# Optimization experiments

Hardware: AMD Instinct MI355X
Metric: run time of the kernel (lower is better)

Reference implementation:

```python
import jax, jax.numpy as jnp
import numpy as np

B, N, K = 2, 1280, 48
C_NODE, C_EDGE, C_OUT = 384, 128, 128
C_BIAS = C_NODE // 2          # 192 (node_dilation=2)
HID = 2 * C_BIAS + C_EDGE     # 512
LN_EPS = 1e-5


def setup_inputs() -> dict:
    key = jax.random.key(0)
    ks = jax.random.split(key, 13)
    w = lambda k, shape: (jax.random.normal(k, shape, jnp.float32) * 0.02)
    return {
        "node_emb": jax.random.normal(ks[0], (B, N, C_NODE), jnp.float32),
        "edge_emb": jax.random.normal(ks[1], (B, N, K, C_EDGE), jnp.float32),
        "E_idx": jax.random.randint(ks[2], (B, N, K), 0, N),
        "Wi": w(ks[3], (C_NODE, C_BIAS)), "bi": jnp.zeros((C_BIAS,), jnp.float32),
        "W1": w(ks[4], (HID, HID)), "b1": jnp.zeros((HID,), jnp.float32),
        "W2": w(ks[5], (HID, HID)), "b2": jnp.zeros((HID,), jnp.float32),
        "Wf": w(ks[6], (HID, C_OUT)), "bf": jnp.zeros((C_OUT,), jnp.float32),
        "gamma": jnp.ones((C_OUT,), jnp.float32),
        "beta": jnp.zeros((C_OUT,), jnp.float32),
    }


def reference(node_emb, edge_emb, E_idx, Wi, bi, W1, b1, W2, b2, Wf, bf, gamma, beta):
    # initial_embed: [B, N, C_NODE] -> [B, N, C_BIAS]
    n = node_emb @ Wi + bi
    # edge_bias[b,i,k] = concat(n[b,i], n[b, E_idx[b,i,k]])  (tile + gather_edges fused)
    nbr = jax.vmap(lambda v, e: v[e])(n, E_idx)                     # [B, N, K, C_BIAS]
    slf = jnp.broadcast_to(n[:, :, None, :], nbr.shape)             # [B, N, K, C_BIAS]
    x = jnp.concatenate([edge_emb, slf, nbr], axis=-1)              # [B, N, K, HID]
    h = jax.nn.relu(x @ W1 + b1)
    h = jax.nn.relu(h @ W2 + b2)
    # final_layer on residual sum, then LayerNorm
    y = (h + x) @ Wf + bf                                           # [B, N, K, C_OUT]
    mu = jnp.mean(y, axis=-1, keepdims=True)
    var = jnp.mean((y - mu) ** 2, axis=-1, keepdims=True)
    return (y - mu) * jax.lax.rsqrt(var + LN_EPS) * gamma + beta
```

## Files before the change

### kernel.cpp

```cpp
#include <hip/hip_runtime.h>
#include <stdint.h>

#define BB    2
#define NN    1280
#define KK    48
#define CN    384
#define CE    128
#define CB    192
#define HID   512
#define CO    128
#define MM    (BB*NN*KK)
#define CH    (MM/2)

typedef __bf16 bf16x8 __attribute__((ext_vector_type(8)));
typedef float  f32x4  __attribute__((ext_vector_type(4)));
typedef unsigned short u16x8 __attribute__((ext_vector_type(8)));

__device__ __forceinline__ unsigned short f2bf(float f) {
  unsigned int i = __builtin_bit_cast(unsigned int, f);
  unsigned int r = (i + 0x7fffu + ((i >> 16) & 1u)) >> 16;
  return (unsigned short)r;
}
__device__ __forceinline__ float bf2f(unsigned short u) {
  unsigned int v = ((unsigned int)u) << 16;
  return __builtin_bit_cast(float, v);
}

__device__ __forceinline__ void gload_lds16(const void* g, void* l) {
  __builtin_amdgcn_global_load_lds(
      (const __attribute__((address_space(1))) void*)g,
      (__attribute__((address_space(3))) void*)l, 16, 0, 0);
}

__device__ __forceinline__ void mfma_tiles(const char* ldsA, const char* ldsB,
                                           int l, int wm, int wn,
                                           f32x4 (&acc)[4][4]) {
#pragma unroll
  for (int kk = 0; kk < 2; ++kk) {
    bf16x8 av[4], bv[4];
#pragma unroll
    for (int t = 0; t < 4; ++t) {
      const int ra = wm * 64 + t * 16 + (l & 15);
      const int ca = (kk * 4 + (l >> 4)) ^ (ra & 7);
      av[t] = *(const bf16x8*)(ldsA + ra * 128 + ca * 16);
      const int rb = wn * 64 + t * 16 + (l & 15);
      const int cb = (kk * 4 + (l >> 4)) ^ (rb & 7);
      bv[t] = *(const bf16x8*)(ldsB + rb * 128 + cb * 16);
    }
#pragma unroll
    for (int mt = 0; mt < 4; ++mt)
#pragma unroll
      for (int nt = 0; nt < 4; ++nt)
        acc[mt][nt] = __builtin_amdgcn_mfma_f32_16x16x32_bf16(av[mt], bv[nt], acc[mt][nt], 0, 0, 0);
  }
}

__global__ void k_transpose_cast(const float* __restrict__ in,
                                 unsigned short* __restrict__ out,
                                 int R, int C) {
  __shared__ float tile[32][33];
  const int c0 = blockIdx.x * 32, r0 = blockIdx.y * 32;
  const int tx = threadIdx.x, ty = threadIdx.y;
#pragma unroll
  for (int dy = 0; dy < 32; dy += 8)
    tile[ty + dy][tx] = in[(size_t)(r0 + ty + dy) * C + c0 + tx];
  __syncthreads();
#pragma unroll
  for (int dy = 0; dy < 32; dy += 8)
    out[(size_t)(c0 + ty + dy) * R + r0 + tx] = f2bf(tile[tx][ty + dy]);
}

__global__ void k_node(const float* __restrict__ node,
                       const float* __restrict__ Wi,
                       const float* __restrict__ bi,
                       unsigned short* __restrict__ nbuf) {
  __shared__ float row[CN];
  const int blk = blockIdx.x;
  const float* src = node + (size_t)blk * CN;
  for (int c = threadIdx.x; c < CN; c += CB) row[c] = src[c];
  __syncthreads();
  const int t = threadIdx.x;
  float acc = bi[t];
#pragma unroll 8
  for (int c = 0; c < CN; ++c) acc += row[c] * Wi[(size_t)c * CB + t];
  nbuf[(size_t)blk * CB + t] = f2bf(acc);
}

__global__ __launch_bounds__(256, 2)
void k_gemm1(const float* __restrict__ edge,
             const unsigned short* __restrict__ nbuf,
             const int* __restrict__ eidx,
             const unsigned short* __restrict__ Wt,
             const float* __restrict__ bias,
             unsigned short* __restrict__ out,
             int mbase, int b) {
  __shared__ char lds[32768];
  char* ldsA = lds;
  char* ldsB = lds + 16384;
  const int flat = blockIdx.x;
  const int xcd = flat & 7;
  const int p = flat >> 3;
  const int m0 = (xcd * 60 + (p >> 2)) * 128;
  const int n0 = (p & 3) * 128;
  const int tid = threadIdx.x;
  const int l = tid & 63;
  const int w = tid >> 6;
  const int wm = w >> 1, wn = w & 1;
  const int sr = l >> 3, pc = l & 7;
  const int lc = pc ^ sr;

  int rr[4], big[4], nbrg[4];
  size_t mg[4];
#pragma unroll
  for (int ii = 0; ii < 4; ++ii) {
    const int r = (w * 4 + ii) * 8 + sr;
    rr[ii] = r;
    const int m = mbase + m0 + r;
    mg[ii] = (size_t)m;
    big[ii] = m / KK;
    nbrg[ii] = b * NN + eidx[m];
  }

  f32x4 acc[4][4];
#pragma unroll
  for (int i = 0; i < 4; ++i)
#pragma unroll
    for (int j = 0; j < 4; ++j) acc[i][j] = (f32x4){0.f, 0.f, 0.f, 0.f};

#pragma unroll
  for (int k0 = 0; k0 < HID; k0 += 64) {
    uint4 rga[4];
    if (k0 < 128) {
#pragma unroll
      for (int ii = 0; ii < 4; ++ii) {
        const float4* ep = (const float4*)(edge + mg[ii] * CE + k0 + lc * 8);
        float4 x0 = ep[0], x1 = ep[1];
        u16x8 pk;
        pk[0] = f2bf(x0.x); pk[1] = f2bf(x0.y); pk[2] = f2bf(x0.z); pk[3] = f2bf(x0.w);
        pk[4] = f2bf(x1.x); pk[5] = f2bf(x1.y); pk[6] = f2bf(x1.z); pk[7] = f2bf(x1.w);
        rga[ii] = __builtin_bit_cast(uint4, pk);
      }
    }
    __syncthreads();
#pragma unroll
    for (int ii = 0; ii < 4; ++ii) {
      const int i = w * 4 + ii;
      gload_lds16(Wt + (size_t)(n0 + rr[ii]) * HID + k0 + lc * 8, ldsB + i * 1024);
      if (k0 < 128) {
        *(uint4*)(ldsA + i * 1024 + l * 16) = rga[ii];
      } else if (k0 < 320) {
        gload_lds16(nbuf + (size_t)big[ii] * CB + (k0 - 128) + lc * 8, ldsA + i * 1024);
      } else {
        gload_lds16(nbuf + (size_t)nbrg[ii] * CB + (k0 - 320) + lc * 8, ldsA + i * 1024);
      }
    }
    __syncthreads();
    mfma_tiles(ldsA, ldsB, l, wm, wn, acc);
  }

  __syncthreads();
  unsigned short* tile = (unsigned short*)lds;
  const int q = l >> 4, cc = l & 15;
#pragma unroll
  for (int nt = 0; nt < 4; ++nt) {
    const int col = wn * 64 + nt * 16 + cc;
    const float bvv = bias[n0 + col];
    const int cn = col >> 3, cb = col & 7;
#pragma unroll
    for (int mt = 0; mt < 4; ++mt) {
      const int r0_ = wm * 64 + mt * 16 + q * 4;
#pragma unroll
      for (int r = 0; r < 4; ++r) {
        float v = acc[mt][nt][r] + bvv;
        v = v > 0.f ? v : 0.f;
        const int row = r0_ + r;
        tile[row * 128 + ((cn ^ (row & 7)) << 3) + cb] = f2bf(v);
      }
    }
  }
  __syncthreads();
#pragma unroll
  for (int i = 0; i < 8; ++i) {
    const int c = i * 256 + tid;
    const int row = c >> 4, cn = c & 15;
    u16x8 vv = *(const u16x8*)(tile + row * 128 + ((cn ^ (row & 7)) << 3));
    *(u16x8*)(out + (size_t)(m0 + row) * HID + n0 + cn * 8) = vv;
  }
}

__global__ __launch_bounds__(256, 2)
void k_gemm2(const unsigned short* __restrict__ A,
             const unsigned short* __restrict__ Wt,
             const float* __restrict__ bias,
             const float* __restrict__ edge,
             const unsigned short* __restrict__ nbuf,
             const int* __restrict__ eidx,
             unsigned short* __restrict__ out,
             int mbase, int b) {
  __shared__ char lds[32768];
  char* ldsA = lds;
  char* ldsB = lds + 16384;
  const int flat = blockIdx.x;
  const int xcd = flat & 7;
  const int p = flat >> 3;
  const int m0 = (xcd * 60 + (p >> 2)) * 128;
  const int n0 = (p & 3) * 128;
  const int tid = threadIdx.x;
  const int l = tid & 63;
  const int w = tid >> 6;
  const int wm = w >> 1, wn = w & 1;
  const int sr = l >> 3, pc = l & 7;
  const int lc = pc ^ sr;

  f32x4 acc[4][4];
#pragma unroll
  for (int i = 0; i < 4; ++i)
#pragma unroll
    for (int j = 0; j < 4; ++j) acc[i][j] = (f32x4){0.f, 0.f, 0.f, 0.f};

#pragma unroll
  for (int k0 = 0; k0 < HID; k0 += 64) {
    __syncthreads();
#pragma unroll
    for (int ii = 0; ii < 4; ++ii) {
      const int i = w * 4 + ii;
      const int r = i * 8 + sr;
      gload_lds16(A  + (size_t)(m0 + r) * HID + k0 + lc * 8, ldsA + i * 1024);
      gload_lds16(Wt + (size_t)(n0 + r) * HID + k0 + lc * 8, ldsB + i * 1024);
    }
    __syncthreads();
    mfma_tiles(ldsA, ldsB, l, wm, wn, acc);
  }

  __syncthreads();
  unsigned short* tile = (unsigned short*)lds;
  const int q = l >> 4, cc = l & 15;
#pragma unroll
  for (int nt = 0; nt < 4; ++nt) {
    const int col = wn * 64 + nt * 16 + cc;
    const float bvv = bias[n0 + col];
    const int cn = col >> 3, cb = col & 7;
#pragma unroll
    for (int mt = 0; mt < 4; ++mt) {
      const int r0_ = wm * 64 + mt * 16 + q * 4;
#pragma unroll
      for (int r = 0; r < 4; ++r) {
        float v = acc[mt][nt][r] + bvv;
        v = v > 0.f ? v : 0.f;
        const int row = r0_ + r;
        tile[row * 128 + ((cn ^ (row & 7)) << 3) + cb] = f2bf(v);
      }
    }
  }
  __syncthreads();
#pragma unroll
  for (int i = 0; i < 8; ++i) {
    const int c = i * 256 + tid;
    const int row = c >> 4, cn = c & 15;
    u16x8 vv = *(const u16x8*)(tile + row * 128 + ((cn ^ (row & 7)) << 3));
    const int m = mbase + m0 + row;
    float rv[8];
    if (n0 == 0) {
      const float4* ep = (const float4*)(edge + (size_t)m * CE + cn * 8);
      float4 x0 = ep[0], x1 = ep[1];
      rv[0] = x0.x; rv[1] = x0.y; rv[2] = x0.z; rv[3] = x0.w;
      rv[4] = x1.x; rv[5] = x1.y; rv[6] = x1.z; rv[7] = x1.w;
    } else if (n0 == 128) {
      u16x8 xv = *(const u16x8*)(nbuf + (size_t)(m / KK) * CB + cn * 8);
#pragma unroll
      for (int j = 0; j < 8; ++j) rv[j] = bf2f(xv[j]);
    } else if (n0 == 256) {
      u16x8 xv;
      if (cn < 8) {
        xv = *(const u16x8*)(nbuf + (size_t)(m / KK) * CB + 128 + cn * 8);
      } else {
        const int e = eidx[m];
        xv = *(const u16x8*)(nbuf + (size_t)(b * NN + e) * CB + cn * 8 - 64);
      }
#pragma unroll
      for (int j = 0; j < 8; ++j) rv[j] = bf2f(xv[j]);
    } else {
      const int e = eidx[m];
      u16x8 xv = *(const u16x8*)(nbuf + (size_t)(b * NN + e) * CB + 64 + cn * 8);
#pragma unroll
      for (int j = 0; j < 8; ++j) rv[j] = bf2f(xv[j]);
    }
#pragma unroll
    for (int j = 0; j < 8; ++j) vv[j] = f2bf(bf2f(vv[j]) + rv[j]);
    *(u16x8*)(out + (size_t)(m0 + row) * HID + n0 + cn * 8) = vv;
  }
}

__global__ __launch_bounds__(256, 2)
void k_final(const unsigned short* __restrict__ A,
             const unsigned short* __restrict__ Wft,
             const float* __restrict__ bias,
             const float* __restrict__ gamma,
             const float* __restrict__ beta,
             float* __restrict__ out) {
  __shared__ char lds[32768];
  char* ldsA = lds;
  char* ldsB = lds + 16384;
  const int m0 = blockIdx.x * 128;
  const int tid = threadIdx.x;
  const int l = tid & 63;
  const int w = tid >> 6;
  const int sr = l >> 3, pc = l & 7;
  const int lc = pc ^ sr;

  f32x4 acc[2][8];
#pragma unroll
  for (int i = 0; i < 2; ++i)
#pragma unroll
    for (int j = 0; j < 8; ++j) acc[i][j] = (f32x4){0.f, 0.f, 0.f, 0.f};

#pragma unroll
  for (int k0 = 0; k0 < HID; k0 += 64) {
    __syncthreads();
#pragma unroll
    for (int ii = 0; ii < 4; ++ii) {
      const int i = w * 4 + ii;
      const int r = i * 8 + sr;
      gload_lds16(A   + (size_t)(m0 + r) * HID + k0 + lc * 8, ldsA + i * 1024);
      gload_lds16(Wft + (size_t)r * HID + k0 + lc * 8,        ldsB + i * 1024);
    }
    __syncthreads();
#pragma unroll
    for (int kk = 0; kk < 2; ++kk) {
      bf16x8 av[2], bv[8];
#pragma unroll
      for (int t = 0; t < 2; ++t) {
        const int ra = w * 32 + t * 16 + (l & 15);
        const int ca = (kk * 4 + (l >> 4)) ^ (ra & 7);
        av[t] = *(const bf16x8*)(ldsA + ra * 128 + ca * 16);
      }
#pragma unroll
      for (int t = 0; t < 8; ++t) {
        const int rb = t * 16 + (l & 15);
        const int cb = (kk * 4 + (l >> 4)) ^ (rb & 7);
        bv[t] = *(const bf16x8*)(ldsB + rb * 128 + cb * 16);
      }
#pragma unroll
      for (int mt = 0; mt < 2; ++mt)
#pragma unroll
        for (int nt = 0; nt < 8; ++nt)
          acc[mt][nt] = __builtin_amdgcn_mfma_f32_16x16x32_bf16(av[mt], bv[nt], acc[mt][nt], 0, 0, 0);
    }
  }

  const int q = l >> 4, cc = l & 15;
  float gg[8], bb[8], bs[8];
#pragma unroll
  for (int j = 0; j < 8; ++j) {
    const int col = j * 16 + cc;
    gg[j] = gamma[col];
    bb[j] = beta[col];
    bs[j] = bias[col];
  }
#pragma unroll
  for (int mt = 0; mt < 2; ++mt) {
#pragma unroll
    for (int r = 0; r < 4; ++r) {
      float s = 0.f, ss = 0.f;
#pragma unroll
      for (int j = 0; j < 8; ++j) {
        const float v = acc[mt][j][r] + bs[j];
        acc[mt][j][r] = v;
        s += v;
        ss += v * v;
      }
#pragma unroll
      for (int mk = 1; mk < 16; mk <<= 1) {
        s  += __shfl_xor(s, mk, 64);
        ss += __shfl_xor(ss, mk, 64);
      }
      const float mu = s * (1.f / 128.f);
      const float var = ss * (1.f / 128.f) - mu * mu;
      const float rstd = rsqrtf(var + 1e-5f);
      const int row = m0 + w * 32 + mt * 16 + q * 4 + r;
#pragma unroll
      for (int j = 0; j < 8; ++j) {
        const float v = (acc[mt][j][r] - mu) * rstd * gg[j] + bb[j];
        out[(size_t)row * CO + j * 16 + cc] = v;
      }
    }
  }
}

#define O_N    ((size_t)0)
#define O_WT1  ((size_t)0x100000)
#define O_WT2  (O_WT1 + (size_t)0x80000)
#define O_WFT  (O_WT2 + (size_t)0x80000)
#define O_H1   ((size_t)0x300000)
#define O_A    (O_H1 + (size_t)CH * HID * 2)

extern "C" void kernel_launch(void* const* d_in, const int* in_sizes, int n_in,
                              void* d_out, int out_size, void* d_ws, size_t ws_size,
                              hipStream_t stream) {
  const float* node  = (const float*)d_in[0];
  const float* edge  = (const float*)d_in[1];
  const int*   eidx  = (const int*)d_in[2];
  const float* Wi    = (const float*)d_in[3];
  const float* bi    = (const float*)d_in[4];
  const float* W1    = (const float*)d_in[5];
  const float* b1    = (const float*)d_in[6];
  const float* W2    = (const float*)d_in[7];
  const float* b2    = (const float*)d_in[8];
  const float* Wf    = (const float*)d_in[9];
  const float* bfv   = (const float*)d_in[10];
  const float* gamma = (const float*)d_in[11];
  const float* beta  = (const float*)d_in[12];
  float* out = (float*)d_out;

  char* ws = (char*)d_ws;
  unsigned short* nbuf = (unsigned short*)(ws + O_N);
  unsigned short* Wt1  = (unsigned short*)(ws + O_WT1);
  unsigned short* Wt2  = (unsigned short*)(ws + O_WT2);
  unsigned short* Wft  = (unsigned short*)(ws + O_WFT);
  unsigned short* h1   = (unsigned short*)(ws + O_H1);
  unsigned short* abuf = (unsigned short*)(ws + O_A);

  k_transpose_cast<<<dim3(HID / 32, HID / 32), dim3(32, 8), 0, stream>>>(W1, Wt1, HID, HID);
  k_transpose_cast<<<dim3(HID / 32, HID / 32), dim3(32, 8), 0, stream>>>(W2, Wt2, HID, HID);
  k_transpose_cast<<<dim3(CO / 32, HID / 32), dim3(32, 8), 0, stream>>>(Wf, Wft, HID, CO);

  k_node<<<BB * NN, CB, 0, stream>>>(node, Wi, bi, nbuf);

  for (int c = 0; c < 2; ++c) {
    k_gemm1<<<(CH / 128) * 4, 256, 0, stream>>>(edge, nbuf, eidx, Wt1, b1, h1, c * CH, c);
    k_gemm2<<<(CH / 128) * 4, 256, 0, stream>>>(h1, Wt2, b2, edge, nbuf, eidx, abuf, c * CH, c);
    k_final<<<CH / 128, 256, 0, stream>>>(abuf, Wft, bfv, gamma, beta, out + (size_t)c * CH * CO);
  }
}
```

Measured before the change: 394.7 us.

## Widen GEMM tiles to full 512-column rows with 512-thread blocks

Both trunk GEMM kernels now have each 512-thread block compute a full 128x512 output tile instead of a 128x128 tile, with eight waves each holding a 64x128 accumulator. The A tile (the gathered edge/node features for GEMM1, h1 for GEMM2) is loaded once per row block rather than four times, which removes the repeated gather and fp32-to-bf16 conversion. The epilogue writes the four 128-column slices through LDS in sequence. In exchange each block uses 80KB of LDS and 128 accumulator registers per lane, so occupancy is lower. The grid is 4x smaller and the XCD-aware block remapping is dropped.

After: 482.4 us. +22.2%, slower.

```diff
diff --git a/kernel.cpp b/kernel.cpp
--- a/kernel.cpp
+++ b/kernel.cpp
@@ -30,29 +30,6 @@
   __builtin_amdgcn_global_load_lds(
       (const __attribute__((address_space(1))) void*)g,
       (__attribute__((address_space(3))) void*)l, 16, 0, 0);
-}
-
-__device__ __forceinline__ void mfma_tiles(const char* ldsA, const char* ldsB,
-                                           int l, int wm, int wn,
-                                           f32x4 (&acc)[4][4]) {
-#pragma unroll
-  for (int kk = 0; kk < 2; ++kk) {
-    bf16x8 av[4], bv[4];
-#pragma unroll
-    for (int t = 0; t < 4; ++t) {
-      const int ra = wm * 64 + t * 16 + (l & 15);
-      const int ca = (kk * 4 + (l >> 4)) ^ (ra & 7);
-      av[t] = *(const bf16x8*)(ldsA + ra * 128 + ca * 16);
-      const int rb = wn * 64 + t * 16 + (l & 15);
-      const int cb = (kk * 4 + (l >> 4)) ^ (rb & 7);
-      bv[t] = *(const bf16x8*)(ldsB + rb * 128 + cb * 16);
-    }
-#pragma unroll
-    for (int mt = 0; mt < 4; ++mt)
-#pragma unroll
-      for (int nt = 0; nt < 4; ++nt)
-        acc[mt][nt] = __builtin_amdgcn_mfma_f32_16x16x32_bf16(av[mt], bv[nt], acc[mt][nt], 0, 0, 0);
-  }
 }
 
 __global__ void k_transpose_cast(const float* __restrict__ in,
@@ -86,7 +63,8 @@
   nbuf[(size_t)blk * CB + t] = f2bf(acc);
 }
 
-__global__ __launch_bounds__(256, 2)
+
+__global__ __launch_bounds__(512, 2)
 void k_gemm1(const float* __restrict__ edge,
              const unsigned short* __restrict__ nbuf,
              const int* __restrict__ eidx,
@@ -94,101 +72,125 @@
              const float* __restrict__ bias,
              unsigned short* __restrict__ out,
              int mbase, int b) {
-  __shared__ char lds[32768];
+  __shared__ char lds[81920];
   char* ldsA = lds;
   char* ldsB = lds + 16384;
-  const int flat = blockIdx.x;
-  const int xcd = flat & 7;
-  const int p = flat >> 3;
-  const int m0 = (xcd * 60 + (p >> 2)) * 128;
-  const int n0 = (p & 3) * 128;
+  const int m0 = blockIdx.x * 128;
   const int tid = threadIdx.x;
   const int l = tid & 63;
   const int w = tid >> 6;
-  const int wm = w >> 1, wn = w & 1;
-  const int sr = l >> 3, pc = l & 7;
-  const int lc = pc ^ sr;
-
-  int rr[4], big[4], nbrg[4];
-  size_t mg[4];
-#pragma unroll
-  for (int ii = 0; ii < 4; ++ii) {
-    const int r = (w * 4 + ii) * 8 + sr;
-    rr[ii] = r;
-    const int m = mbase + m0 + r;
-    mg[ii] = (size_t)m;
-    big[ii] = m / KK;
-    nbrg[ii] = b * NN + eidx[m];
-  }
-
-  f32x4 acc[4][4];
+  const int wm = w >> 2, wn = w & 3;
+  const int kg = l >> 4, lr = l & 15;
+  const int srow = tid >> 3;
+  const int pc = tid & 7;
+  const int lc = pc ^ (srow & 7);
+
+  int bigA[2], nbrA[2];
+  size_t mA[2];
+#pragma unroll
+  for (int i = 0; i < 2; ++i) {
+    const int m = mbase + m0 + i * 64 + srow;
+    mA[i] = (size_t)m;
+    bigA[i] = m / KK;
+    nbrA[i] = b * NN + eidx[m];
+  }
+
+  f32x4 acc[4][8];
 #pragma unroll
   for (int i = 0; i < 4; ++i)
 #pragma unroll
-    for (int j = 0; j < 4; ++j) acc[i][j] = (f32x4){0.f, 0.f, 0.f, 0.f};
+    for (int j = 0; j < 8; ++j) acc[i][j] = (f32x4){0.f, 0.f, 0.f, 0.f};
 
 #pragma unroll
   for (int k0 = 0; k0 < HID; k0 += 64) {
-    uint4 rga[4];
+    uint4 rga[2];
     if (k0 < 128) {
 #pragma unroll
-      for (int ii = 0; ii < 4; ++ii) {
-        const float4* ep = (const float4*)(edge + mg[ii] * CE + k0 + lc * 8);
+      for (int i = 0; i < 2; ++i) {
+        const float4* ep = (const float4*)(edge + mA[i] * CE + k0 + lc * 8);
         float4 x0 = ep[0], x1 = ep[1];
         u16x8 pk;
         pk[0] = f2bf(x0.x); pk[1] = f2bf(x0.y); pk[2] = f2bf(x0.z); pk[3] = f2bf(x0.w);
         pk[4] = f2bf(x1.x); pk[5] = f2bf(x1.y); pk[6] = f2bf(x1.z); pk[7] = f2bf(x1.w);
-        rga[ii] = __builtin_bit_cast(uint4, pk);
-      }
-    }
-    __syncthreads();
-#pragma unroll
-    for (int ii = 0; ii < 4; ++ii) {
-      const int i = w * 4 + ii;
-      gload_lds16(Wt + (size_t)(n0 + rr[ii]) * HID + k0 + lc * 8, ldsB + i * 1024);
+        rga[i] = __builtin_bit_cast(uint4, pk);
+      }
+    }
+    __syncthreads();
+#pragma unroll
+    for (int j = 0; j < 8; ++j)
+      gload_lds16(Wt + (size_t)(j * 64 + srow) * HID + k0 + lc * 8,
+                  ldsB + j * 8192 + tid * 16);
+#pragma unroll
+    for (int i = 0; i < 2; ++i) {
       if (k0 < 128) {
-        *(uint4*)(ldsA + i * 1024 + l * 16) = rga[ii];
+        *(uint4*)(ldsA + i * 8192 + tid * 16) = rga[i];
       } else if (k0 < 320) {
-        gload_lds16(nbuf + (size_t)big[ii] * CB + (k0 - 128) + lc * 8, ldsA + i * 1024);
+        gload_lds16(nbuf + (size_t)bigA[i] * CB + (k0 - 128) + lc * 8,
+                    ldsA + i * 8192 + tid * 16);
       } else {
-        gload_lds16(nbuf + (size_t)nbrg[ii] * CB + (k0 - 320) + lc * 8, ldsA + i * 1024);
-      }
-    }
-    __syncthreads();
-    mfma_tiles(ldsA, ldsB, l, wm, wn, acc);
-  }
-
-  __syncthreads();
+        gload_lds16(nbuf + (size_t)nbrA[i] * CB + (k0 - 320) + lc * 8,
+                    ldsA + i * 8192 + tid * 16);
+      }
+    }
+    __syncthreads();
+#pragma unroll
+    for (int kk = 0; kk < 2; ++kk) {
+      bf16x8 av[4], bv[8];
+#pragma unroll
+      for (int t = 0; t < 4; ++t) {
+        const int ra = wm * 64 + t * 16 + lr;
+        const int ca = (kk * 4 + kg) ^ (ra & 7);
+        av[t] = *(const bf16x8*)(ldsA + ra * 128 + ca * 16);
+      }
+#pragma unroll
+      for (int u = 0; u < 8; ++u) {
+        const int rb = wn * 128 + u * 16 + lr;
+        const int cb = (kk * 4 + kg) ^ (rb & 7);
+        bv[u] = *(const bf16x8*)(ldsB + rb * 128 + cb * 16);
+      }
+#pragma unroll
+      for (int t = 0; t < 4; ++t)
+#pragma unroll
+        for (int u = 0; u < 8; ++u)
+          acc[t][u] = __builtin_amdgcn_mfma_f32_16x16x32_bf16(av[t], bv[u], acc[t][u], 0, 0, 0);
+    }
+  }
+
   unsigned short* tile = (unsigned short*)lds;
-  const int q = l >> 4, cc = l & 15;
-#pragma unroll
-  for (int nt = 0; nt < 4; ++nt) {
-    const int col = wn * 64 + nt * 16 + cc;
-    const float bvv = bias[n0 + col];
-    const int cn = col >> 3, cb = col & 7;
-#pragma unroll
-    for (int mt = 0; mt < 4; ++mt) {
-      const int r0_ = wm * 64 + mt * 16 + q * 4;
-#pragma unroll
-      for (int r = 0; r < 4; ++r) {
-        float v = acc[mt][nt][r] + bvv;
-        v = v > 0.f ? v : 0.f;
-        const int row = r0_ + r;
-        tile[row * 128 + ((cn ^ (row & 7)) << 3) + cb] = f2bf(v);
-      }
-    }
-  }
-  __syncthreads();
-#pragma unroll
-  for (int i = 0; i < 8; ++i) {
-    const int c = i * 256 + tid;
-    const int row = c >> 4, cn = c & 15;
-    u16x8 vv = *(const u16x8*)(tile + row * 128 + ((cn ^ (row & 7)) << 3));
-    *(u16x8*)(out + (size_t)(m0 + row) * HID + n0 + cn * 8) = vv;
-  }
-}
-
-__global__ __launch_bounds__(256, 2)
+#pragma unroll
+  for (int q = 0; q < 4; ++q) {
+    __syncthreads();
+    if (wn == q) {
+#pragma unroll
+      for (int u = 0; u < 8; ++u) {
+        const int col = u * 16 + lr;
+        const float bvv = bias[q * 128 + col];
+        const int cn = col >> 3, cb = col & 7;
+#pragma unroll
+        for (int t = 0; t < 4; ++t) {
+          const int r0_ = wm * 64 + t * 16 + kg * 4;
+#pragma unroll
+          for (int r = 0; r < 4; ++r) {
+            float v = acc[t][u][r] + bvv;
+            v = v > 0.f ? v : 0.f;
+            const int row = r0_ + r;
+            tile[row * 128 + ((cn ^ (row & 7)) << 3) + cb] = f2bf(v);
+          }
+        }
+      }
+    }
+    __syncthreads();
+#pragma unroll
+    for (int i = 0; i < 4; ++i) {
+      const int c = i * 512 + tid;
+      const int row = c >> 4, cn = c & 15;
+      u16x8 vv = *(const u16x8*)(tile + row * 128 + ((cn ^ (row & 7)) << 3));
+      *(u16x8*)(out + (size_t)(m0 + row) * HID + q * 128 + cn * 8) = vv;
+    }
+  }
+}
+
+__global__ __launch_bounds__(512, 2)
 void k_gemm2(const unsigned short* __restrict__ A,
              const unsigned short* __restrict__ Wt,
              const float* __restrict__ bias,
@@ -197,97 +199,120 @@
              const int* __restrict__ eidx,
              unsigned short* __restrict__ out,
              int mbase, int b) {
-  __shared__ char lds[32768];
+  __shared__ char lds[81920];
   char* ldsA = lds;
   char* ldsB = lds + 16384;
-  const int flat = blockIdx.x;
-  const int xcd = flat & 7;
-  const int p = flat >> 3;
-  const int m0 = (xcd * 60 + (p >> 2)) * 128;
-  const int n0 = (p & 3) * 128;
+  const int m0 = blockIdx.x * 128;
   const int tid = threadIdx.x;
   const int l = tid & 63;
   const int w = tid >> 6;
-  const int wm = w >> 1, wn = w & 1;
-  const int sr = l >> 3, pc = l & 7;
-  const int lc = pc ^ sr;
-
-  f32x4 acc[4][4];
+  const int wm = w >> 2, wn = w & 3;
+  const int kg = l >> 4, lr = l & 15;
+  const int srow = tid >> 3;
+  const int pc = tid & 7;
+  const int lc = pc ^ (srow & 7);
+
+  f32x4 acc[4][8];
 #pragma unroll
   for (int i = 0; i < 4; ++i)
 #pragma unroll
-    for (int j = 0; j < 4; ++j) acc[i][j] = (f32x4){0.f, 0.f, 0.f, 0.f};
+    for (int j = 0; j < 8; ++j) acc[i][j] = (f32x4){0.f, 0.f, 0.f, 0.f};
 
 #pragma unroll
   for (int k0 = 0; k0 < HID; k0 += 64) {
     __syncthreads();
 #pragma unroll
-    for (int ii = 0; ii < 4; ++ii) {
-      const int i = w * 4 + ii;
-      const int r = i * 8 + sr;
-      gload_lds16(A  + (size_t)(m0 + r) * HID + k0 + lc * 8, ldsA + i * 1024);
-      gload_lds16(Wt + (size_t)(n0 + r) * HID + k0 + lc * 8, ldsB + i * 1024);
-    }
-    __syncthreads();
-    mfma_tiles(ldsA, ldsB, l, wm, wn, acc);
-  }
-
-  __syncthreads();
+    for (int j = 0; j < 8; ++j)
+      gload_lds16(Wt + (size_t)(j * 64 + srow) * HID + k0 + lc * 8,
+                  ldsB + j * 8192 + tid * 16);
+#pragma unroll
+    for (int i = 0; i < 2; ++i)
+      gload_lds16(A + (size_t)(m0 + i * 64 + srow) * HID + k0 + lc * 8,
+                  ldsA + i * 8192 + tid * 16);
+    __syncthreads();
+#pragma unroll
+    for (int kk = 0; kk < 2; ++kk) {
+      bf16x8 av[4], bv[8];
+#pragma unroll
+      for (int t = 0; t < 4; ++t) {
+        const int ra = wm * 64 + t * 16 + lr;
+        const int ca = (kk * 4 + kg) ^ (ra & 7);
+        av[t] = *(const bf16x8*)(ldsA + ra * 128 + ca * 16);
+      }
+#pragma unroll
+      for (int u = 0; u < 8; ++u) {
+        const int rb = wn * 128 + u * 16 + lr;
+        const int cb = (kk * 4 + kg) ^ (rb & 7);
+        bv[u] = *(const bf16x8*)(ldsB + rb * 128 + cb * 16);
+      }
+#pragma unroll
+      for (int t = 0; t < 4; ++t)
+#pragma unroll
+        for (int u = 0; u < 8; ++u)
+          acc[t][u] = __builtin_amdgcn_mfma_f32_16x16x32_bf16(av[t], bv[u], acc[t][u], 0, 0, 0);
+    }
+  }
+
   unsigned short* tile = (unsigned short*)lds;
-  const int q = l >> 4, cc = l & 15;
-#pragma unroll
-  for (int nt = 0; nt < 4; ++nt) {
-    const int col = wn * 64 + nt * 16 + cc;
-    const float bvv = bias[n0 + col];
-    const int cn = col >> 3, cb = col & 7;
-#pragma unroll
-    for (int mt = 0; mt < 4; ++mt) {
-      const int r0_ = wm * 64 + mt * 16 + q * 4;
-#pragma unroll
-      for (int r = 0; r < 4; ++r) {
-        float v = acc[mt][nt][r] + bvv;
-        v = v > 0.f ? v : 0.f;
-        const int row = r0_ + r;
-        tile[row * 128 + ((cn ^ (row & 7)) << 3) + cb] = f2bf(v);
-      }
-    }
-  }
-  __syncthreads();
-#pragma unroll
-  for (int i = 0; i < 8; ++i) {
-    const int c = i * 256 + tid;
-    const int row = c >> 4, cn = c & 15;
-    u16x8 vv = *(const u16x8*)(tile + row * 128 + ((cn ^ (row & 7)) << 3));
-    const int m = mbase + m0 + row;
-    float rv[8];
-    if (n0 == 0) {
-      const float4* ep = (const float4*)(edge + (size_t)m * CE + cn * 8);
-      float4 x0 = ep[0], x1 = ep[1];
-      rv[0] = x0.x; rv[1] = x0.y; rv[2] = x0.z; rv[3] = x0.w;
-      rv[4] = x1.x; rv[5] = x1.y; rv[6] = x1.z; rv[7] = x1.w;
-    } else if (n0 == 128) {
-      u16x8 xv = *(const u16x8*)(nbuf + (size_t)(m / KK) * CB + cn * 8);
-#pragma unroll
-      for (int j = 0; j < 8; ++j) rv[j] = bf2f(xv[j]);
-    } else if (n0 == 256) {
-      u16x8 xv;
-      if (cn < 8) {
-        xv = *(const u16x8*)(nbuf + (size_t)(m / KK) * CB + 128 + cn * 8);
+#pragma unroll
+  for (int q = 0; q < 4; ++q) {
+    __syncthreads();
+    if (wn == q) {
+#pragma unroll
+      for (int u = 0; u < 8; ++u) {
+        const int col = u * 16 + lr;
+        const float bvv = bias[q * 128 + col];
+        const int cn = col >> 3, cb = col & 7;
+#pragma unroll
+        for (int t = 0; t < 4; ++t) {
+          const int r0_ = wm * 64 + t * 16 + kg * 4;
+#pragma unroll
+          for (int r = 0; r < 4; ++r) {
+            float v = acc[t][u][r] + bvv;
+            v = v > 0.f ? v : 0.f;
+            const int row = r0_ + r;
+            tile[row * 128 + ((cn ^ (row & 7)) << 3) + cb] = f2bf(v);
+          }
+        }
+      }
+    }
+    __syncthreads();
+#pragma unroll
+    for (int i = 0; i < 4; ++i) {
+      const int c = i * 512 + tid;
+      const int row = c >> 4, cn = c & 15;
+      u16x8 vv = *(const u16x8*)(tile + row * 128 + ((cn ^ (row & 7)) << 3));
+      const int m = mbase + m0 + row;
+      float rv[8];
+      if (q == 0) {
+        const float4* ep = (const float4*)(edge + (size_t)m * CE + cn * 8);
+        float4 x0 = ep[0], x1 = ep[1];
+        rv[0] = x0.x; rv[1] = x0.y; rv[2] = x0.z; rv[3] = x0.w;
+        rv[4] = x1.x; rv[5] = x1.y; rv[6] = x1.z; rv[7] = x1.w;
+      } else if (q == 1) {
+        u16x8 xv = *(const u16x8*)(nbuf + (size_t)(m / KK) * CB + cn * 8);
+#pragma unroll
+        for (int j = 0; j < 8; ++j) rv[j] = bf2f(xv[j]);
+      } else if (q == 2) {
+        u16x8 xv;
+        if (cn < 8) {
+          xv = *(const u16x8*)(nbuf + (size_t)(m / KK) * CB + 128 + cn * 8);
+        } else {
+          const int e = eidx[m];
+          xv = *(const u16x8*)(nbuf + (size_t)(b * NN + e) * CB + cn * 8 - 64);
+        }
+#pragma unroll
+        for (int j = 0; j < 8; ++j) rv[j] = bf2f(xv[j]);
       } else {
         const int e = eidx[m];
-        xv = *(const u16x8*)(nbuf + (size_t)(b * NN + e) * CB + cn * 8 - 64);
-      }
-#pragma unroll
-      for (int j = 0; j < 8; ++j) rv[j] = bf2f(xv[j]);
-    } else {
-      const int e = eidx[m];
-      u16x8 xv = *(const u16x8*)(nbuf + (size_t)(b * NN + e) * CB + 64 + cn * 8);
-#pragma unroll
-      for (int j = 0; j < 8; ++j) rv[j] = bf2f(xv[j]);
-    }
-#pragma unroll
-    for (int j = 0; j < 8; ++j) vv[j] = f2bf(bf2f(vv[j]) + rv[j]);
-    *(u16x8*)(out + (size_t)(m0 + row) * HID + n0 + cn * 8) = vv;
+        u16x8 xv = *(const u16x8*)(nbuf + (size_t)(b * NN + e) * CB + 64 + cn * 8);
+#pragma unroll
+        for (int j = 0; j < 8; ++j) rv[j] = bf2f(xv[j]);
+      }
+#pragma unroll
+      for (int j = 0; j < 8; ++j) vv[j] = f2bf(bf2f(vv[j]) + rv[j]);
+      *(u16x8*)(out + (size_t)(m0 + row) * HID + q * 128 + cn * 8) = vv;
+    }
   }
 }
 
@@ -427,8 +452,8 @@
   k_node<<<BB * NN, CB, 0, stream>>>(node, Wi, bi, nbuf);
 
   for (int c = 0; c < 2; ++c) {
-    k_gemm1<<<(CH / 128) * 4, 256, 0, stream>>>(edge, nbuf, eidx, Wt1, b1, h1, c * CH, c);
-    k_gemm2<<<(CH / 128) * 4, 256, 0, stream>>>(h1, Wt2, b2, edge, nbuf, eidx, abuf, c * CH, c);
+    k_gemm1<<<CH / 128, 512, 0, stream>>>(edge, nbuf, eidx, Wt1, b1, h1, c * CH, c);
+    k_gemm2<<<CH / 128, 512, 0, stream>>>(h1, Wt2, b2, edge, nbuf, eidx, abuf, c * CH, c);
     k_final<<<CH / 128, 256, 0, stream>>>(abuf, Wft, bfv, gamma, beta, out + (size_t)c * CH * CO);
   }
 }
```
